# Optimization experiments

Measured on AMD Instinct MI355X. Metric: run time of the kernel, lower is better.

## Reference

```python
import jax, jax.numpy as jnp
import numpy as np

N, F, H, F_ = 8192, 256, 2, 64
NEG_MASK = -1e10
LEAKY_SLOPE = 0.2


def setup_inputs() -> dict:
    key = jax.random.key(0)
    k0, k1, k2, k3 = jax.random.split(key, 4)
    X = jax.random.normal(k0, (N, F), jnp.float32)
    A = (jax.random.uniform(k1, (N, N)) < 0.01).astype(jnp.float32)
    A = jnp.maximum(A, jnp.eye(N, dtype=jnp.float32))
    W = jax.random.normal(k2, (H, F, F_), jnp.float32) * (1.0 / np.sqrt(F))
    b = jnp.zeros((H, F_), jnp.float32)
    a = jax.random.normal(k3, (H, F_), jnp.float32) * 0.1
    return {"X": X, "A": A, "W": W, "b": b, "a": a}


def reference(X, A, W, b, a):
    # per-head projected features: [H, N, F_]
    feats = jnp.einsum('nf,hfo->hno', X, W)
    # score[h,i,j] = sum_o feats[h,i,o] * feats[h,j,o] * a[h,o]
    # (identical math to Dot(axes=-1)([X_0*X_1, a^T]) without the [N,N,F_] tensor)
    scores = jnp.einsum('hno,hmo->hnm', feats * a[:, None, :], feats)
    scores = jax.nn.leaky_relu(scores, negative_slope=LEAKY_SLOPE)
    scores = scores + NEG_MASK * (1.0 - A)  # adjacency mask (broadcast over heads)
    attn = jax.nn.softmax(scores, axis=-1)  # [H, N, N]
    # dropout_rate=0 -> identity at inference
    out = jnp.einsum('hnm,hmo->hno', attn, feats) + b[:, None, :]  # [H, N, F_]
    out = jnp.transpose(out, (1, 0, 2)).reshape(X.shape[0], H * F_)  # concat heads
    return jax.nn.relu(out)
```

## Files before the change

kernel.cpp:

```cpp
#include <hip/hip_runtime.h>

#define NN 8192
#define FIN 256
#define FO 64
#define CAP 192

__global__ __launch_bounds__(256) void feats_kernel(
    const float* __restrict__ X,
    const float* __restrict__ W,
    float* __restrict__ feats)
{
    __shared__ float Ws[128*FO];
    __shared__ float Xs[32*132];
    const int h = blockIdx.y;
    const int row0 = blockIdx.x * 32;
    const int t = threadIdx.x;
    const int rg = t >> 4;
    const int c0 = (t & 15) << 2;
    float acc0[4] = {0.f,0.f,0.f,0.f};
    float acc1[4] = {0.f,0.f,0.f,0.f};

    for (int kp = 0; kp < 2; ++kp){
        const int kb = kp * 128;
        const float* Wh = W + h*FIN*FO + kb*FO;
        #pragma unroll
        for (int it=0; it<8; ++it){
            int flat = (it*256 + t)*4;
            *(float4*)&Ws[flat] = *(const float4*)&Wh[flat];
        }
        #pragma unroll
        for (int it=0; it<4; ++it){
            int flat = (it*256 + t)*4;
            int r = flat >> 7, f0 = flat & 127;
            *(float4*)&Xs[r*132 + f0] = *(const float4*)&X[(size_t)(row0+r)*FIN + kb + f0];
        }
        __syncthreads();
        const float* xp0 = &Xs[(rg*2+0)*132];
        const float* xp1 = &Xs[(rg*2+1)*132];
        #pragma unroll 4
        for (int k=0; k<128; ++k){
            float x0 = xp0[k], x1 = xp1[k];
            float4 w4 = *(const float4*)&Ws[k*FO + c0];
            acc0[0]=fmaf(x0,w4.x,acc0[0]); acc0[1]=fmaf(x0,w4.y,acc0[1]);
            acc0[2]=fmaf(x0,w4.z,acc0[2]); acc0[3]=fmaf(x0,w4.w,acc0[3]);
            acc1[0]=fmaf(x1,w4.x,acc1[0]); acc1[1]=fmaf(x1,w4.y,acc1[1]);
            acc1[2]=fmaf(x1,w4.z,acc1[2]); acc1[3]=fmaf(x1,w4.w,acc1[3]);
        }
        __syncthreads();
    }
    float* o0 = feats + ((size_t)(row0 + rg*2 + 0)*2 + h)*FO + c0;
    float* o1 = feats + ((size_t)(row0 + rg*2 + 1)*2 + h)*FO + c0;
    *(float4*)o0 = make_float4(acc0[0],acc0[1],acc0[2],acc0[3]);
    *(float4*)o1 = make_float4(acc1[0],acc1[1],acc1[2],acc1[3]);
}

__global__ __launch_bounds__(512) void gat_kernel(
    const float* __restrict__ A,
    const float* __restrict__ feats,
    const float* __restrict__ av,
    const float* __restrict__ bv,
    float* __restrict__ out)
{
    __shared__ int   nsh[CAP];
    __shared__ float s0[CAP], s1[CAP];
    __shared__ float part[4*128];
    __shared__ float red[2];
    __shared__ int   s_c;

    const int i = blockIdx.x, t = threadIdx.x;
    const int l  = t & 63;
    const int wv = t >> 6;
    const int gi = t >> 5, l32 = t & 31;

    float4 qa = *(const float4*)&av[l32*4];
    float4 qf = *(const float4*)&feats[(size_t)i*128 + l32*4];
    const float4 q4 = make_float4(qf.x*qa.x, qf.y*qa.y, qf.z*qa.z, qf.w*qa.w);

    if (t == 0) s_c = 0;
    __syncthreads();

    const float4* Arow4 = (const float4*)(A + (size_t)i*NN);
    float4 v[4];
    #pragma unroll
    for (int r=0; r<4; ++r) v[r] = Arow4[r*512 + t];

    const unsigned long long ltmask = (1ull << l) - 1ull;
    #pragma unroll
    for (int r=0; r<4; ++r){
        float vals[4] = {v[r].x, v[r].y, v[r].z, v[r].w};
        #pragma unroll
        for (int e=0; e<4; ++e){
            bool nz = (vals[e] != 0.0f);
            unsigned long long m = __ballot(nz);
            int base = 0;
            if (l == 0) base = atomicAdd(&s_c, __popcll(m));
            base = __shfl(base, 0, 64);
            if (nz){
                int p = base + __popcll(m & ltmask);
                if (p < CAP) nsh[p] = (r*512 + t)*4 + e;
            }
        }
    }
    __syncthreads();
    const int n = min(s_c, CAP);

    for (int k=gi; k<n; k+=16){
        int j = nsh[k];
        float4 f4 = *(const float4*)&feats[(size_t)j*128 + l32*4];
        float d = f4.x*q4.x + f4.y*q4.y + f4.z*q4.z + f4.w*q4.w;
        d += __shfl_xor(d, 1, 64);
        d += __shfl_xor(d, 2, 64);
        d += __shfl_xor(d, 4, 64);
        d += __shfl_xor(d, 8, 64);
        d = (d >= 0.f) ? d : 0.2f*d;
        if (l32 == 0)  s0[k] = d;
        if (l32 == 16) s1[k] = d;
    }
    __syncthreads();

    if (wv < 2){
        float* ss = wv ? s1 : s0;
        float m = -1e30f;
        for (int k=l; k<n; k+=64) m = fmaxf(m, ss[k]);
        #pragma unroll
        for (int off=32; off; off>>=1) m = fmaxf(m, __shfl_xor(m, off, 64));
        float sum = 0.f;
        for (int k=l; k<n; k+=64){ float p = __expf(ss[k]-m); ss[k] = p; sum += p; }
        #pragma unroll
        for (int off=32; off; off>>=1) sum += __shfl_xor(sum, off, 64);
        if (l == 0) red[wv] = sum;
    }
    __syncthreads();

    const int op = t & 127, g = t >> 7;
    const float* ps = (op >= 64) ? s1 : s0;
    float acc = 0.f;
    for (int k=g; k<n; k+=4){
        int j = nsh[k];
        acc = fmaf(ps[k], feats[(size_t)j*128 + op], acc);
    }
    part[g*128 + op] = acc;
    __syncthreads();

    if (t < 128){
        float num = part[t] + part[128+t] + part[256+t] + part[384+t];
        float val = num / red[t>>6] + bv[t];
        out[(size_t)i*128 + t] = fmaxf(val, 0.f);
    }
}

extern "C" void kernel_launch(void* const* d_in, const int* in_sizes, int n_in,
                              void* d_out, int out_size, void* d_ws, size_t ws_size,
                              hipStream_t stream) {
    const float* X = (const float*)d_in[0];
    const float* A = (const float*)d_in[1];
    const float* W = (const float*)d_in[2];
    const float* b = (const float*)d_in[3];
    const float* a = (const float*)d_in[4];
    float* out = (float*)d_out;

    float* feats = (float*)d_ws;

    feats_kernel<<<dim3(NN/32, 2), 256, 0, stream>>>(X, W, feats);
    gat_kernel  <<<dim3(NN),       512, 0, stream>>>(A, feats, a, b, out);
}
```

Measured before the change: 428.5 us.

## Batch ballot compaction, use nontemporal A loads, and unroll gather loops

Result: faster. 391.9 us (-8.6%).

```diff
diff --git a/kernel.cpp b/kernel.cpp
--- a/kernel.cpp
+++ b/kernel.cpp
@@ -4,6 +4,8 @@
 #define FIN 256
 #define FO 64
 #define CAP 192
+
+typedef float nf4 __attribute__((ext_vector_type(4)));
 
 __global__ __launch_bounds__(256) void feats_kernel(
     const float* __restrict__ X,
@@ -63,7 +65,7 @@
 {
     __shared__ int   nsh[CAP];
     __shared__ float s0[CAP], s1[CAP];
-    __shared__ float part[4*128];
+    __shared__ float part[8*128];
     __shared__ float red[2];
     __shared__ int   s_c;
 
@@ -79,42 +81,52 @@
     if (t == 0) s_c = 0;
     __syncthreads();
 
-    const float4* Arow4 = (const float4*)(A + (size_t)i*NN);
-    float4 v[4];
+    const nf4* Arow4 = (const nf4*)(A + (size_t)i*NN);
+    nf4 v[4];
     #pragma unroll
-    for (int r=0; r<4; ++r) v[r] = Arow4[r*512 + t];
+    for (int r=0; r<4; ++r) v[r] = __builtin_nontemporal_load(&Arow4[r*512 + t]);
 
     const unsigned long long ltmask = (1ull << l) - 1ull;
     #pragma unroll
     for (int r=0; r<4; ++r){
-        float vals[4] = {v[r].x, v[r].y, v[r].z, v[r].w};
-        #pragma unroll
-        for (int e=0; e<4; ++e){
-            bool nz = (vals[e] != 0.0f);
-            unsigned long long m = __ballot(nz);
-            int base = 0;
-            if (l == 0) base = atomicAdd(&s_c, __popcll(m));
-            base = __shfl(base, 0, 64);
-            if (nz){
-                int p = base + __popcll(m & ltmask);
-                if (p < CAP) nsh[p] = (r*512 + t)*4 + e;
-            }
-        }
+        unsigned long long m0 = __ballot(v[r].x != 0.0f);
+        unsigned long long m1 = __ballot(v[r].y != 0.0f);
+        unsigned long long m2 = __ballot(v[r].z != 0.0f);
+        unsigned long long m3 = __ballot(v[r].w != 0.0f);
+        int p0 = __popcll(m0), p1 = __popcll(m1), p2 = __popcll(m2), p3 = __popcll(m3);
+        int base = 0;
+        if (l == 0) base = atomicAdd(&s_c, p0+p1+p2+p3);
+        base = __shfl(base, 0, 64);
+        const int colb = (r*512 + t)*4;
+        if ((m0>>l)&1){ int p = base + __popcll(m0 & ltmask); if (p<CAP) nsh[p] = colb;   } base += p0;
+        if ((m1>>l)&1){ int p = base + __popcll(m1 & ltmask); if (p<CAP) nsh[p] = colb+1; } base += p1;
+        if ((m2>>l)&1){ int p = base + __popcll(m2 & ltmask); if (p<CAP) nsh[p] = colb+2; } base += p2;
+        if ((m3>>l)&1){ int p = base + __popcll(m3 & ltmask); if (p<CAP) nsh[p] = colb+3; }
     }
     __syncthreads();
     const int n = min(s_c, CAP);
 
-    for (int k=gi; k<n; k+=16){
-        int j = nsh[k];
-        float4 f4 = *(const float4*)&feats[(size_t)j*128 + l32*4];
-        float d = f4.x*q4.x + f4.y*q4.y + f4.z*q4.z + f4.w*q4.w;
-        d += __shfl_xor(d, 1, 64);
-        d += __shfl_xor(d, 2, 64);
-        d += __shfl_xor(d, 4, 64);
-        d += __shfl_xor(d, 8, 64);
-        d = (d >= 0.f) ? d : 0.2f*d;
-        if (l32 == 0)  s0[k] = d;
-        if (l32 == 16) s1[k] = d;
+    for (int k0 = gi*4; k0 < n; k0 += 64){
+        const int kn = min(4, n - k0);
+        float4 f[4];
+        #pragma unroll
+        for (int u=0; u<4; ++u){
+            int j = (u < kn) ? nsh[k0+u] : i;
+            f[u] = *(const float4*)&feats[(size_t)j*128 + l32*4];
+        }
+        #pragma unroll
+        for (int u=0; u<4; ++u){
+            float d = f[u].x*q4.x + f[u].y*q4.y + f[u].z*q4.z + f[u].w*q4.w;
+            d += __shfl_xor(d, 1, 64);
+            d += __shfl_xor(d, 2, 64);
+            d += __shfl_xor(d, 4, 64);
+            d += __shfl_xor(d, 8, 64);
+            d = (d >= 0.f) ? d : 0.2f*d;
+            if (u < kn){
+                if (l32 == 0)  s0[k0+u] = d;
+                if (l32 == 16) s1[k0+u] = d;
+            }
+        }
     }
     __syncthreads();
 
@@ -132,18 +144,35 @@
     }
     __syncthreads();
 
-    const int op = t & 127, g = t >> 7;
-    const float* ps = (op >= 64) ? s1 : s0;
-    float acc = 0.f;
-    for (int k=g; k<n; k+=4){
+    const int g8 = t >> 6;
+    const int o2 = (t & 63) * 2;
+    const float* ps = (o2 >= 64) ? s1 : s0;
+    float2 acc = make_float2(0.f, 0.f);
+    int k = g8;
+    for (; k + 24 < n; k += 32){
+        int j0 = nsh[k], j1 = nsh[k+8], j2 = nsh[k+16], j3 = nsh[k+24];
+        float2 f0 = *(const float2*)&feats[(size_t)j0*128 + o2];
+        float2 f1 = *(const float2*)&feats[(size_t)j1*128 + o2];
+        float2 f2 = *(const float2*)&feats[(size_t)j2*128 + o2];
+        float2 f3 = *(const float2*)&feats[(size_t)j3*128 + o2];
+        float p0 = ps[k], p1 = ps[k+8], p2 = ps[k+16], p3 = ps[k+24];
+        acc.x = fmaf(p0, f0.x, acc.x); acc.y = fmaf(p0, f0.y, acc.y);
+        acc.x = fmaf(p1, f1.x, acc.x); acc.y = fmaf(p1, f1.y, acc.y);
+        acc.x = fmaf(p2, f2.x, acc.x); acc.y = fmaf(p2, f2.y, acc.y);
+        acc.x = fmaf(p3, f3.x, acc.x); acc.y = fmaf(p3, f3.y, acc.y);
+    }
+    for (; k < n; k += 8){
         int j = nsh[k];
-        acc = fmaf(ps[k], feats[(size_t)j*128 + op], acc);
+        float2 f = *(const float2*)&feats[(size_t)j*128 + o2];
+        float p = ps[k];
+        acc.x = fmaf(p, f.x, acc.x); acc.y = fmaf(p, f.y, acc.y);
     }
-    part[g*128 + op] = acc;
+    *(float2*)&part[g8*128 + o2] = acc;
     __syncthreads();
 
     if (t < 128){
-        float num = part[t] + part[128+t] + part[256+t] + part[384+t];
+        float num = part[t]       + part[128+t] + part[256+t] + part[384+t]
+                  + part[512+t]   + part[640+t] + part[768+t] + part[896+t];
         float val = num / red[t>>6] + bv[t];
         out[(size_t)i*128 + t] = fmaxf(val, 0.f);
     }
```

## Process one attention row per wavefront with sync-free neighbor compaction

Applied to the files above, without the earlier changes.

New measurement: 429.0 us. About the same (+0.1%).

```diff
diff --git a/kernel.cpp b/kernel.cpp
--- a/kernel.cpp
+++ b/kernel.cpp
@@ -4,6 +4,9 @@
 #define FIN 256
 #define FO 64
 #define CAP 192
+
+typedef float nf4 __attribute__((ext_vector_type(4)));
+typedef unsigned long long ull;
 
 __global__ __launch_bounds__(256) void feats_kernel(
     const float* __restrict__ X,
@@ -48,105 +51,117 @@
         }
         __syncthreads();
     }
-    float* o0 = feats + ((size_t)(row0 + rg*2 + 0)*2 + h)*FO + c0;
-    float* o1 = feats + ((size_t)(row0 + rg*2 + 1)*2 + h)*FO + c0;
+    float* o0 = feats + (size_t)(row0 + rg*2 + 0)*128 + h*FO + c0;
+    float* o1 = feats + (size_t)(row0 + rg*2 + 1)*128 + h*FO + c0;
     *(float4*)o0 = make_float4(acc0[0],acc0[1],acc0[2],acc0[3]);
     *(float4*)o1 = make_float4(acc1[0],acc1[1],acc1[2],acc1[3]);
 }
 
-__global__ __launch_bounds__(512) void gat_kernel(
+__global__ __launch_bounds__(256) void gat_kernel(
     const float* __restrict__ A,
     const float* __restrict__ feats,
     const float* __restrict__ av,
     const float* __restrict__ bv,
     float* __restrict__ out)
 {
-    __shared__ int   nsh[CAP];
-    __shared__ float s0[CAP], s1[CAP];
-    __shared__ float part[4*128];
-    __shared__ float red[2];
-    __shared__ int   s_c;
+    __shared__ int   jsh[4][CAP];
+    __shared__ float psh[4][2][CAP];
+    __shared__ float qsh[4][128];
 
-    const int i = blockIdx.x, t = threadIdx.x;
-    const int l  = t & 63;
-    const int wv = t >> 6;
-    const int gi = t >> 5, l32 = t & 31;
+    const int t = threadIdx.x, w = t >> 6, l = t & 63;
+    const int i = blockIdx.x*4 + w;
+    const int h  = l & 1,  m  = l >> 1;
+    const int ha = l >> 5, oa = (l & 31) * 2;
+    const ull ltmask = (1ull << l) - 1ull;
 
-    float4 qa = *(const float4*)&av[l32*4];
-    float4 qf = *(const float4*)&feats[(size_t)i*128 + l32*4];
-    const float4 q4 = make_float4(qf.x*qa.x, qf.y*qa.y, qf.z*qa.z, qf.w*qa.w);
+    qsh[w][l]      = feats[(size_t)i*128 + l]      * av[l];
+    qsh[w][64 + l] = feats[(size_t)i*128 + 64 + l] * av[64 + l];
 
-    if (t == 0) s_c = 0;
-    __syncthreads();
-
-    const float4* Arow4 = (const float4*)(A + (size_t)i*NN);
-    float4 v[4];
+    const nf4* Ar = (const nf4*)(A + (size_t)i*NN);
+    int cnt = 0;
     #pragma unroll
-    for (int r=0; r<4; ++r) v[r] = Arow4[r*512 + t];
-
-    const unsigned long long ltmask = (1ull << l) - 1ull;
-    #pragma unroll
-    for (int r=0; r<4; ++r){
-        float vals[4] = {v[r].x, v[r].y, v[r].z, v[r].w};
+    for (int s=0; s<4; ++s){
+        nf4 v[8];
         #pragma unroll
-        for (int e=0; e<4; ++e){
-            bool nz = (vals[e] != 0.0f);
-            unsigned long long m = __ballot(nz);
-            int base = 0;
-            if (l == 0) base = atomicAdd(&s_c, __popcll(m));
-            base = __shfl(base, 0, 64);
-            if (nz){
-                int p = base + __popcll(m & ltmask);
-                if (p < CAP) nsh[p] = (r*512 + t)*4 + e;
-            }
+        for (int r=0; r<8; ++r) v[r] = __builtin_nontemporal_load(&Ar[(s*8+r)*64 + l]);
+        #pragma unroll
+        for (int r=0; r<8; ++r){
+            ull m0 = __ballot(v[r].x != 0.0f);
+            ull m1 = __ballot(v[r].y != 0.0f);
+            ull m2 = __ballot(v[r].z != 0.0f);
+            ull m3 = __ballot(v[r].w != 0.0f);
+            const int colb = ((s*8+r)*64 + l)*4;
+            if ((m0>>l)&1){ int p = cnt + __popcll(m0 & ltmask); if (p<CAP) jsh[w][p] = colb;   }
+            cnt += __popcll(m0);
+            if ((m1>>l)&1){ int p = cnt + __popcll(m1 & ltmask); if (p<CAP) jsh[w][p] = colb+1; }
+            cnt += __popcll(m1);
+            if ((m2>>l)&1){ int p = cnt + __popcll(m2 & ltmask); if (p<CAP) jsh[w][p] = colb+2; }
+            cnt += __popcll(m2);
+            if ((m3>>l)&1){ int p = cnt + __popcll(m3 & ltmask); if (p<CAP) jsh[w][p] = colb+3; }
+            cnt += __popcll(m3);
         }
     }
-    __syncthreads();
-    const int n = min(s_c, CAP);
+    const int n = min(cnt, CAP);
+    __threadfence_block();
 
-    for (int k=gi; k<n; k+=16){
-        int j = nsh[k];
-        float4 f4 = *(const float4*)&feats[(size_t)j*128 + l32*4];
-        float d = f4.x*q4.x + f4.y*q4.y + f4.z*q4.z + f4.w*q4.w;
-        d += __shfl_xor(d, 1, 64);
-        d += __shfl_xor(d, 2, 64);
-        d += __shfl_xor(d, 4, 64);
-        d += __shfl_xor(d, 8, 64);
-        d = (d >= 0.f) ? d : 0.2f*d;
-        if (l32 == 0)  s0[k] = d;
-        if (l32 == 16) s1[k] = d;
+    float sr[6];
+    const int nr = (n + 31) >> 5;
+    float mx = -1e30f;
+    const float4* qh = (const float4*)&qsh[w][h*64];
+    for (int r=0; r<nr; ++r){
+        int k = r*32 + m;
+        bool valid = k < n;
+        int j = valid ? jsh[w][k] : i;
+        const float4* fj = (const float4*)&feats[(size_t)j*128 + h*64];
+        float s = 0.f;
+        #pragma unroll
+        for (int u=0; u<16; ++u){
+            float4 f = fj[u], qq = qh[u];
+            s += f.x*qq.x + f.y*qq.y + f.z*qq.z + f.w*qq.w;
+        }
+        s = (s >= 0.f) ? s : 0.2f*s;
+        if (!valid) s = -1e30f;
+        sr[r] = s;
+        mx = fmaxf(mx, s);
     }
-    __syncthreads();
+    #pragma unroll
+    for (int off=2; off<64; off<<=1) mx = fmaxf(mx, __shfl_xor(mx, off, 64));
+    float sum = 0.f;
+    for (int r=0; r<nr; ++r){ float p = __expf(sr[r] - mx); sr[r] = p; sum += p; }
+    #pragma unroll
+    for (int off=2; off<64; off<<=1) sum += __shfl_xor(sum, off, 64);
+    const float inv = 1.0f / sum;
+    for (int r=0; r<nr; ++r){
+        int k = r*32 + m;
+        if (k < n) psh[w][h][k] = sr[r] * inv;
+    }
+    __threadfence_block();
 
-    if (wv < 2){
-        float* ss = wv ? s1 : s0;
-        float m = -1e30f;
-        for (int k=l; k<n; k+=64) m = fmaxf(m, ss[k]);
-        #pragma unroll
-        for (int off=32; off; off>>=1) m = fmaxf(m, __shfl_xor(m, off, 64));
-        float sum = 0.f;
-        for (int k=l; k<n; k+=64){ float p = __expf(ss[k]-m); ss[k] = p; sum += p; }
-        #pragma unroll
-        for (int off=32; off; off>>=1) sum += __shfl_xor(sum, off, 64);
-        if (l == 0) red[wv] = sum;
+    const float* ph = psh[w][ha];
+    const int fo = ha*64 + oa;
+    float2 acc = make_float2(0.f, 0.f);
+    int k = 0;
+    for (; k+3 < n; k += 4){
+        int j0 = jsh[w][k], j1 = jsh[w][k+1], j2 = jsh[w][k+2], j3 = jsh[w][k+3];
+        float2 f0 = *(const float2*)&feats[(size_t)j0*128 + fo];
+        float2 f1 = *(const float2*)&feats[(size_t)j1*128 + fo];
+        float2 f2 = *(const float2*)&feats[(size_t)j2*128 + fo];
+        float2 f3 = *(const float2*)&feats[(size_t)j3*128 + fo];
+        float p0 = ph[k], p1 = ph[k+1], p2 = ph[k+2], p3 = ph[k+3];
+        acc.x = fmaf(p0, f0.x, acc.x); acc.y = fmaf(p0, f0.y, acc.y);
+        acc.x = fmaf(p1, f1.x, acc.x); acc.y = fmaf(p1, f1.y, acc.y);
+        acc.x = fmaf(p2, f2.x, acc.x); acc.y = fmaf(p2, f2.y, acc.y);
+        acc.x = fmaf(p3, f3.x, acc.x); acc.y = fmaf(p3, f3.y, acc.y);
     }
-    __syncthreads();
-
-    const int op = t & 127, g = t >> 7;
-    const float* ps = (op >= 64) ? s1 : s0;
-    float acc = 0.f;
-    for (int k=g; k<n; k+=4){
-        int j = nsh[k];
-        acc = fmaf(ps[k], feats[(size_t)j*128 + op], acc);
+    for (; k < n; ++k){
+        int j = jsh[w][k];
+        float2 f = *(const float2*)&feats[(size_t)j*128 + fo];
+        float p = ph[k];
+        acc.x = fmaf(p, f.x, acc.x); acc.y = fmaf(p, f.y, acc.y);
     }
-    part[g*128 + op] = acc;
-    __syncthreads();
-
-    if (t < 128){
-        float num = part[t] + part[128+t] + part[256+t] + part[384+t];
-        float val = num / red[t>>6] + bv[t];
-        out[(size_t)i*128 + t] = fmaxf(val, 0.f);
-    }
+    float2 bb = *(const float2*)&bv[fo];
+    float2 o2 = make_float2(fmaxf(acc.x + bb.x, 0.f), fmaxf(acc.y + bb.y, 0.f));
+    *(float2*)&out[(size_t)i*128 + fo] = o2;
 }
 
 extern "C" void kernel_launch(void* const* d_in, const int* in_sizes, int n_in,
@@ -162,5 +177,5 @@
     float* feats = (float*)d_ws;
 
     feats_kernel<<<dim3(NN/32, 2), 256, 0, stream>>>(X, W, feats);
-    gat_kernel  <<<dim3(NN),       512, 0, stream>>>(A, feats, a, b, out);
+    gat_kernel  <<<dim3(NN/4),     256, 0, stream>>>(A, feats, a, b, out);
 }
```
